# Kernel tuning notes

Measured on AMD Instinct MI355X. Metric: run time of the kernel, lower is better.

The kernel has to match this reference:

```python
import jax, jax.numpy as jnp
import numpy as np

B, T, A, C = 8, 512, 512, 8
D, NHEAD, FF, L = 256, 8, 1024, 3
DEC_FF = 512
V = 32          # categorical cardinality per feature (tables have 1+V rows, row 0 = padding)
NEG = -1e9      # finite stand-in for -inf: exp underflows to 0 exactly, masked rows are zeroed anyway


def layer_norm(x, g, b, eps=1e-5):
    m = jnp.mean(x, axis=-1, keepdims=True)
    v = jnp.mean(jnp.square(x - m), axis=-1, keepdims=True)
    return (x - m) * jax.lax.rsqrt(v + eps) * g + b


def mha(q_in, k_in, v_in, wq, wk, wv, wo, nhead, mask=None):
    b, _, dm = q_in.shape
    dh = dm // nhead
    # faithful to the original torch code: .view(B, nhead, -1, d_head) with NO transpose
    q = (q_in @ wq).reshape(b, nhead, -1, dh)
    k = (k_in @ wk).reshape(b, nhead, -1, dh)
    v = (v_in @ wv).reshape(b, nhead, -1, dh)
    u = jnp.einsum('bhqd,bhkd->bhqk', q, k) / float(np.sqrt(dh))
    if mask is not None:
        m = mask[:, None]  # [B,1,q,k] (broadcast)
        attn = jax.nn.softmax(jnp.where(m, NEG, u), axis=-1)
        attn = jnp.where(m, 0.0, attn)
    else:
        attn = jax.nn.softmax(u, axis=-1)
    return jnp.einsum('bhqk,bhkd->bhqd', attn, v).reshape(b, -1, dm) @ wo


def embed(x, tables, wo, bo):
    # all features categorical: Embedder sums per-feature embeddings of (1 + x), then a Linear
    nf = x.shape[-1]
    e = tables[jnp.arange(nf), 1 + x]  # [B,N,nf,D]
    return jnp.sum(e, axis=2) @ wo + bo


def encoder(x, mask, wq, wk, wv, wo, w1, b1, w2, b2, g1, be1, g2, be2):
    for i in range(wq.shape[0]):
        x = layer_norm(x + mha(x, x, x, wq[i], wk[i], wv[i], wo[i], NHEAD, mask), g1[i], be1[i])
        x = layer_norm(x + jax.nn.relu(x @ w1[i] + b1[i]) @ w2[i] + b2[i], g2[i], be2[i])
    return x


def forward(tasks, agents, indices, P):
    (emb_t, emb_t_wo, emb_t_bo, emb_a, emb_a_wo, emb_a_bo,
     et_wq, et_wk, et_wv, et_wo, et_w1, et_b1, et_w2, et_b2, et_g1, et_be1, et_g2, et_be2,
     ea_wq, ea_wk, ea_wv, ea_wo, ea_w1, ea_b1, ea_w2, ea_b2, ea_g1, ea_be1, ea_g2, ea_be2,
     de_wq, de_wk, de_wv, de_wo, de_w1, de_b1, de_w2, de_b2, de_g1, de_be1, de_g2, de_be2,
     do_wq, do_wk) = P
    padding_mask = jnp.all(tasks == -1, axis=-1)[:, None, :]  # [B,1,T]
    # _get_mask: scatter assigned task indices (slot 0 absorbs the -1 padding)
    b_idx = jnp.arange(B)[:, None, None]
    a_idx = jnp.arange(A)[None, :, None]
    am = jnp.zeros((B, A, 1 + T), jnp.bool_).at[b_idx, a_idx, 1 + indices].set(True)
    assignment_mask = jnp.any(am[..., 1:], axis=1, keepdims=True)      # [B,1,T]
    full_mask = jnp.all(indices != -1, axis=-1, keepdims=True)         # [B,A,1]
    mask = jnp.swapaxes(assignment_mask | padding_mask | full_mask, -1, -2)  # [B,T,A]
    ht = encoder(embed(tasks, emb_t, emb_t_wo, emb_t_bo), padding_mask,
                 et_wq, et_wk, et_wv, et_wo, et_w1, et_b1, et_w2, et_b2, et_g1, et_be1, et_g2, et_be2)
    ha = encoder(embed(agents, emb_a, emb_a_wo, emb_a_bo), padding_mask,
                 ea_wq, ea_wk, ea_wv, ea_wo, ea_w1, ea_b1, ea_w2, ea_b2, ea_g1, ea_be1, ea_g2, ea_be2)
    # decoder (x=ha, h=ht): queries are the task stream, keys/values the agent stream
    h = layer_norm(ht + mha(ht, ha, ha, de_wq, de_wk, de_wv, de_wo, NHEAD, mask), de_g1, de_be1)
    h = layer_norm(h + jax.nn.relu(h @ de_w1 + de_b1) @ de_w2 + de_b2, de_g2, de_be2)
    # output attention (nhead=1, d_head=D); mean over the singleton head dim is identity
    scores = jnp.einsum('btd,bad->bta', h @ do_wq, ha @ do_wk) / float(np.sqrt(D))
    probs = 8.0 * jnp.tanh(scores)                                     # [B,T,A]
    p = jax.nn.softmax(jnp.where(mask, NEG, probs), axis=-1)
    p = jnp.where(mask, 0.0, p)
    return jnp.swapaxes(p, -1, -2)                                     # [B,A,T]


def setup_inputs():
    key = jax.random.key(0)
    kc = iter(jax.random.split(key, 64))
    def w(*shape):
        return jax.random.normal(next(kc), shape, jnp.float32) * 0.05
    def table(nf):
        t = jax.random.normal(next(kc), (nf, 1 + V, D), jnp.float32) * 0.05
        return t.at[:, 0].set(0.0)  # padding_idx=0
    inp = {
        'tasks': jax.random.randint(next(kc), (B, T, 4), 0, V, jnp.int32),
        'agents': jax.random.randint(next(kc), (B, A, 2), 0, V, jnp.int32),
        'indices': jax.random.randint(next(kc), (B, A, C), 0, T + 1, jnp.int32) - 1,  # in [-1, T-1]
        'emb_t': table(4), 'emb_t_wo': w(D, D), 'emb_t_bo': jnp.zeros((D,), jnp.float32),
        'emb_a': table(2), 'emb_a_wo': w(D, D), 'emb_a_bo': jnp.zeros((D,), jnp.float32),
    }
    for pre in ('et', 'ea'):
        inp[pre + '_wq'] = w(L, D, D); inp[pre + '_wk'] = w(L, D, D)
        inp[pre + '_wv'] = w(L, D, D); inp[pre + '_wo'] = w(L, D, D)
        inp[pre + '_w1'] = w(L, D, FF); inp[pre + '_b1'] = jnp.zeros((L, FF), jnp.float32)
        inp[pre + '_w2'] = w(L, FF, D); inp[pre + '_b2'] = jnp.zeros((L, D), jnp.float32)
        inp[pre + '_g1'] = jnp.ones((L, D), jnp.float32); inp[pre + '_be1'] = jnp.zeros((L, D), jnp.float32)
        inp[pre + '_g2'] = jnp.ones((L, D), jnp.float32); inp[pre + '_be2'] = jnp.zeros((L, D), jnp.float32)
    inp['de_wq'] = w(D, D); inp['de_wk'] = w(D, D); inp['de_wv'] = w(D, D); inp['de_wo'] = w(D, D)
    inp['de_w1'] = w(D, DEC_FF); inp['de_b1'] = jnp.zeros((DEC_FF,), jnp.float32)
    inp['de_w2'] = w(DEC_FF, D); inp['de_b2'] = jnp.zeros((D,), jnp.float32)
    inp['de_g1'] = jnp.ones((D,), jnp.float32); inp['de_be1'] = jnp.zeros((D,), jnp.float32)
    inp['de_g2'] = jnp.ones((D,), jnp.float32); inp['de_be2'] = jnp.zeros((D,), jnp.float32)
    inp['do_wq'] = w(D, D); inp['do_wk'] = w(D, D)
    return inp


def reference(tasks, agents, indices, emb_t, emb_t_wo, emb_t_bo, emb_a, emb_a_wo, emb_a_bo,
              et_wq, et_wk, et_wv, et_wo, et_w1, et_b1, et_w2, et_b2, et_g1, et_be1, et_g2, et_be2,
              ea_wq, ea_wk, ea_wv, ea_wo, ea_w1, ea_b1, ea_w2, ea_b2, ea_g1, ea_be1, ea_g2, ea_be2,
              de_wq, de_wk, de_wv, de_wo, de_w1, de_b1, de_w2, de_b2, de_g1, de_be1, de_g2, de_be2,
              do_wq, do_wk):
    P = (emb_t, emb_t_wo, emb_t_bo, emb_a, emb_a_wo, emb_a_bo,
         et_wq, et_wk, et_wv, et_wo, et_w1, et_b1, et_w2, et_b2, et_g1, et_be1, et_g2, et_be2,
         ea_wq, ea_wk, ea_wv, ea_wo, ea_w1, ea_b1, ea_w2, ea_b2, ea_g1, ea_be1, ea_g2, ea_be2,
         de_wq, de_wk, de_wv, de_wo, de_w1, de_b1, de_w2, de_b2, de_g1, de_be1, de_g2, de_be2,
         do_wq, do_wk)
    return forward(tasks, agents, indices, P)
```

## Files before the change

kernel.cpp:

```cpp
#include <hip/hip_runtime.h>
#include <hip/hip_bf16.h>

constexpr int CB = 8;
constexpr int CT = 512;
constexpr int CA = 512;
constexpr int CC = 8;
constexpr int CD = 256;
constexpr float NEGV = -1.0e9f;

typedef __attribute__((ext_vector_type(8))) short bf16x8;
typedef __attribute__((ext_vector_type(4))) float f32x4;

__device__ inline short f2bf(float f) {
  uint32_t u = __float_as_uint(f);
  uint32_t r = (u + 0x7FFFu + ((u >> 16) & 1u)) >> 16;
  return (short)r;
}

__global__ void mask_prep_kernel(const int* __restrict__ tasks,
                                 const int* __restrict__ indices,
                                 int* __restrict__ asgn, int* __restrict__ fullm,
                                 int* __restrict__ padm) {
  int i = blockIdx.x * blockDim.x + threadIdx.x;
  if (i >= CB * CT) return;
  asgn[i] = 0;
  const int* tp = tasks + i * 4;
  padm[i] = (tp[0] == -1) && (tp[1] == -1) && (tp[2] == -1) && (tp[3] == -1);
  const int* ip = indices + i * CC;
  int full = 1;
#pragma unroll
  for (int c = 0; c < CC; ++c) full &= (ip[c] != -1);
  fullm[i] = full;
}

__global__ void mask_assign_kernel(const int* __restrict__ indices, int* __restrict__ asgn) {
  int i = blockIdx.x * blockDim.x + threadIdx.x;
  if (i >= CB * CA * CC) return;
  int b = i / (CA * CC);
  int idx = indices[i];
  if (idx >= 0) asgn[b * CT + idx] = 1;
}

struct TDesc { const float* src; short* dst; int K; int N; int tbase; };
struct TArgs { TDesc d[46]; int nd; };

__global__ __launch_bounds__(256) void trans_kernel(TArgs a) {
  __shared__ short Ts[64][72];
  const int bid = blockIdx.x;
  int w = 0;
#pragma unroll 1
  for (int i = 1; i < a.nd; ++i)
    if (a.d[i].tbase <= bid) w = i;
  const TDesc de = a.d[w];
  const int ti = bid - de.tbase;
  const int ntn = de.N >> 6;
  const int n0 = (ti % ntn) * 64, k0 = (ti / ntn) * 64;
  const int t = threadIdx.x;
  const int kk = t >> 4, c4 = (t & 15) * 4;
#pragma unroll
  for (int r = 0; r < 4; ++r) {
    float4 v = *(const float4*)(de.src + (size_t)(k0 + kk + r * 16) * de.N + n0 + c4);
    Ts[c4 + 0][kk + r * 16] = f2bf(v.x);
    Ts[c4 + 1][kk + r * 16] = f2bf(v.y);
    Ts[c4 + 2][kk + r * 16] = f2bf(v.z);
    Ts[c4 + 3][kk + r * 16] = f2bf(v.w);
  }
  __syncthreads();
  const int n = t >> 3, k8 = (t & 7) * 8;
#pragma unroll
  for (int r = 0; r < 2; ++r)
    *(bf16x8*)(de.dst + (size_t)(n0 + n + r * 32) * de.K + k0 + k8) =
        *(bf16x8*)&Ts[n + r * 32][k8];
}

__global__ void embed2_kernel(const int* __restrict__ tasks, const int* __restrict__ agents,
                              const float* __restrict__ tab_t, const float* __restrict__ tab_a,
                              short* __restrict__ out) {
  int row = blockIdx.x;
  int lane = threadIdx.x;
  const int* tp;
  const float* table;
  int nf;
  short* dst;
  if (row < 4096) {
    tp = tasks + row * 4; table = tab_t; nf = 4; dst = out + (size_t)row * CD;
  } else {
    int r = row - 4096;
    tp = agents + r * 2; table = tab_a; nf = 2; dst = out + 1048576 + (size_t)r * CD;
  }
  float4 acc = make_float4(0.f, 0.f, 0.f, 0.f);
  for (int f = 0; f < nf; ++f) {
    int t = 1 + tp[f];
    float4 v = *(const float4*)(table + ((size_t)f * 33 + t) * CD + lane * 4);
    acc.x += v.x; acc.y += v.y; acc.z += v.z; acc.w += v.w;
  }
  short4 o;
  o.x = f2bf(acc.x); o.y = f2bf(acc.y); o.z = f2bf(acc.z); o.w = f2bf(acc.w);
  *(short4*)(dst + lane * 4) = o;
}

__device__ __forceinline__ void ln_row(float* x, const float* res, const float* g,
                                       const float* b, short* xb, int row, int lane) {
  float4 xv = *(const float4*)(x + (size_t)row * CD + lane * 4);
  float4 rv = *(const float4*)(res + (size_t)row * CD + lane * 4);
  float v0 = xv.x + rv.x, v1 = xv.y + rv.y, v2 = xv.z + rv.z, v3 = xv.w + rv.w;
  float s = v0 + v1 + v2 + v3;
  float s2 = v0 * v0 + v1 * v1 + v2 * v2 + v3 * v3;
#pragma unroll
  for (int off = 32; off >= 1; off >>= 1) {
    s += __shfl_xor(s, off);
    s2 += __shfl_xor(s2, off);
  }
  float mean = s * (1.0f / CD);
  float var = s2 * (1.0f / CD) - mean * mean;
  float rstd = rsqrtf(var + 1e-5f);
  float4 gv = *(const float4*)(g + lane * 4);
  float4 bv = *(const float4*)(b + lane * 4);
  float4 o;
  o.x = (v0 - mean) * rstd * gv.x + bv.x;
  o.y = (v1 - mean) * rstd * gv.y + bv.y;
  o.z = (v2 - mean) * rstd * gv.z + bv.z;
  o.w = (v3 - mean) * rstd * gv.w + bv.w;
  *(float4*)(x + (size_t)row * CD + lane * 4) = o;
  short4 ob;
  ob.x = f2bf(o.x); ob.y = f2bf(o.y); ob.z = f2bf(o.z); ob.w = f2bf(o.w);
  *(short4*)(xb + (size_t)row * CD + lane * 4) = ob;
}

__global__ __launch_bounds__(256) void ln_add1_kernel(
    float* __restrict__ x, const float* __restrict__ res,
    const float* __restrict__ g, const float* __restrict__ b, short* __restrict__ xb) {
  int row = blockIdx.x * 4 + (threadIdx.x >> 6);
  ln_row(x, res, g, b, xb, row, threadIdx.x & 63);
}

__global__ __launch_bounds__(256) void ln_add2_kernel(
    float* __restrict__ x0, const float* __restrict__ r0, const float* __restrict__ g0,
    const float* __restrict__ b0, short* __restrict__ s0,
    float* __restrict__ x1, const float* __restrict__ r1, const float* __restrict__ g1,
    const float* __restrict__ b1, short* __restrict__ s1) {
  int row = blockIdx.x * 4 + (threadIdx.x >> 6);
  int lane = threadIdx.x & 63;
  if (row < 4096) ln_row(x0, r0, g0, b0, s0, row, lane);
  else ln_row(x1, r1, g1, b1, s1, row - 4096, lane);
}

template <int CMODE, bool BIAS, bool RELU>
__device__ __forceinline__ void gemm_body(
    const short* __restrict__ Ab, const short* __restrict__ Bb,
    const float* __restrict__ bias, float* __restrict__ Cf, short* __restrict__ Cbf,
    int Ndim, int Kdim, int bm, int bn) {
  __shared__ __align__(16) short As[2][128 * 64];
  __shared__ __align__(16) short Bs[2][64 * 64];
  const int t = threadIdx.x;
  const int lane = t & 63, wave = t >> 6;
  const int wm = wave * 32;
  const int fr = lane & 15, fs = lane >> 4;
  const int fr7 = fr & 7;

  const int srow = t >> 3;
  const int lc = (t & 7) ^ (srow & 7);
  const short* Asrc = Ab + (size_t)(bm + srow) * Kdim + lc * 8;
  const short* Bsrc = Bb + (size_t)(bn + srow) * Kdim + lc * 8;

  f32x4 acc[2][4] = {};

  auto stage = [&](int buf, int k0) {
#pragma unroll
    for (int r = 0; r < 4; ++r)
      __builtin_amdgcn_global_load_lds(
          (const __attribute__((address_space(1))) void*)(Asrc + (size_t)(r * 32) * Kdim + k0),
          (__attribute__((address_space(3))) void*)(&As[buf][r * 2048 + wave * 512]),
          16, 0, 0);
#pragma unroll
    for (int r = 0; r < 2; ++r)
      __builtin_amdgcn_global_load_lds(
          (const __attribute__((address_space(1))) void*)(Bsrc + (size_t)(r * 32) * Kdim + k0),
          (__attribute__((address_space(3))) void*)(&Bs[buf][r * 2048 + wave * 512]),
          16, 0, 0);
  };

  stage(0, 0);
  __syncthreads();
  int buf = 0;
#pragma unroll 1
  for (int k0 = 0; k0 < Kdim; k0 += 64) {
    if (k0 + 64 < Kdim) stage(buf ^ 1, k0 + 64);
    const short* A0 = &As[buf][(wm + fr) * 64];
    const short* A1 = &As[buf][(wm + 16 + fr) * 64];
    const short* B0 = &Bs[buf][fr * 64];
    const short* B1 = &Bs[buf][(16 + fr) * 64];
    const short* B2 = &Bs[buf][(32 + fr) * 64];
    const short* B3 = &Bs[buf][(48 + fr) * 64];
#pragma unroll
    for (int kk = 0; kk < 2; ++kk) {
      const int co = (((kk * 4) + fs) ^ fr7) * 8;
      bf16x8 a0 = *(bf16x8*)(A0 + co);
      bf16x8 a1 = *(bf16x8*)(A1 + co);
      bf16x8 bf0 = *(bf16x8*)(B0 + co);
      bf16x8 bf1 = *(bf16x8*)(B1 + co);
      bf16x8 bf2 = *(bf16x8*)(B2 + co);
      bf16x8 bf3 = *(bf16x8*)(B3 + co);
      acc[0][0] = __builtin_amdgcn_mfma_f32_16x16x32_bf16(a0, bf0, acc[0][0], 0, 0, 0);
      acc[0][1] = __builtin_amdgcn_mfma_f32_16x16x32_bf16(a0, bf1, acc[0][1], 0, 0, 0);
      acc[0][2] = __builtin_amdgcn_mfma_f32_16x16x32_bf16(a0, bf2, acc[0][2], 0, 0, 0);
      acc[0][3] = __builtin_amdgcn_mfma_f32_16x16x32_bf16(a0, bf3, acc[0][3], 0, 0, 0);
      acc[1][0] = __builtin_amdgcn_mfma_f32_16x16x32_bf16(a1, bf0, acc[1][0], 0, 0, 0);
      acc[1][1] = __builtin_amdgcn_mfma_f32_16x16x32_bf16(a1, bf1, acc[1][1], 0, 0, 0);
      acc[1][2] = __builtin_amdgcn_mfma_f32_16x16x32_bf16(a1, bf2, acc[1][2], 0, 0, 0);
      acc[1][3] = __builtin_amdgcn_mfma_f32_16x16x32_bf16(a1, bf3, acc[1][3], 0, 0, 0);
    }
    __syncthreads();
    buf ^= 1;
  }

#pragma unroll
  for (int fi = 0; fi < 2; ++fi)
#pragma unroll
    for (int fj = 0; fj < 4; ++fj) {
      int row0 = bm + wm + fi * 16 + fs * 4;
      int col = bn + fj * 16 + fr;
      float bv = BIAS ? bias[col] : 0.0f;
#pragma unroll
      for (int r = 0; r < 4; ++r) {
        float v = acc[fi][fj][r] + bv;
        if (RELU) v = fmaxf(v, 0.0f);
        if (CMODE == 0 || CMODE == 2) Cf[(size_t)(row0 + r) * Ndim + col] = v;
        if (CMODE == 1 || CMODE == 2) Cbf[(size_t)(row0 + r) * Ndim + col] = f2bf(v);
      }
    }
}

struct GArgs {
  const short* A[8];
  const short* Bm[8];
  const float* bias[8];
  float* Cf[8];
  short* Cb[8];
  int Ndim, Kdim;
};

template <int CMODE, bool BIAS, bool RELU>
__global__ __launch_bounds__(256) void mgemm_kernel(GArgs ga) {
  int z = blockIdx.z;
  gemm_body<CMODE, BIAS, RELU>(ga.A[z], ga.Bm[z], ga.bias[z], ga.Cf[z], ga.Cb[z],
                               ga.Ndim, ga.Kdim, blockIdx.x * 128, blockIdx.y * 64);
}

template <int MODE>
__global__ __launch_bounds__(512) void mattn_kernel(
    const short* __restrict__ qb, const short* __restrict__ kb, const short* __restrict__ vb,
    short* __restrict__ ob,
    const int* __restrict__ asgn, const int* __restrict__ fullm, const int* __restrict__ padm) {
  __shared__ short Ks[512][40];
  __shared__ short Vt[32][520];
  __shared__ short Pb[8][16][40];
  __shared__ unsigned int mwords[16];
  const int bh = blockIdx.x;
  const int b = (bh >> 3) & 7;
  const size_t base = (size_t)bh * (512 * 32);
  const int tid = threadIdx.x;

#pragma unroll
  for (int r = 0; r < 4; ++r) {
    int i = r * 512 + tid;
    int row = i >> 2, seg = (i & 3) * 8;
    *(bf16x8*)&Ks[row][seg] = *(const bf16x8*)(kb + base + row * 32 + seg);
  }
  {
    int d = tid & 31, g = tid >> 5;
#pragma unroll
    for (int r = 0; r < 8; ++r) {
      int key0 = (r * 16 + g) * 4;
      const short* vp = vb + base + (size_t)key0 * 32 + d;
      unsigned short p0 = (unsigned short)vp[0];
      unsigned short p1 = (unsigned short)vp[32];
      unsigned short p2 = (unsigned short)vp[64];
      unsigned short p3 = (unsigned short)vp[96];
      int lo = ((int)p0) | (((int)p1) << 16);
      int hi = ((int)p2) | (((int)p3) << 16);
      *(int2*)&Vt[d][key0] = make_int2(lo, hi);
    }
  }
  if (tid < 16) {
    unsigned w = 0;
    for (int tl = 0; tl < 32; ++tl) {
      int key = tl * 16 + tid;
      int m = (MODE == 0) ? padm[b * CT + key] : fullm[b * CA + key];
      w |= ((unsigned)(m != 0)) << tl;
    }
    mwords[tid] = w;
  }
  __syncthreads();

  const int wave = tid >> 6, lane = tid & 63;
  const int fr = lane & 15, fs = lane >> 4;
  const int q0 = blockIdx.y * 128 + wave * 16;
  const int q = q0 + fr;

  bf16x8 qf = *(const bf16x8*)(qb + base + (size_t)q * 32 + fs * 8);

  unsigned qmbits = 0;
  if (MODE == 1) {
    int qm = asgn[b * CT + q] | padm[b * CT + q];
    qmbits = qm ? 0xFFFFFFFFu : 0u;
  }
  unsigned mw[4];
#pragma unroll
  for (int g = 0; g < 4; ++g) mw[g] = mwords[4 * fs + g] | qmbits;

  f32x4 s[32];
#pragma unroll
  for (int tl = 0; tl < 32; ++tl) {
    bf16x8 kf = *(bf16x8*)&Ks[tl * 16 + fr][fs * 8];
    f32x4 z = {0.f, 0.f, 0.f, 0.f};
    s[tl] = __builtin_amdgcn_mfma_f32_16x16x32_bf16(kf, qf, z, 0, 0, 0);
  }
  const float sc = 0.17677669529663687f;
  float mx = -3.0e38f;
#pragma unroll
  for (int tl = 0; tl < 32; ++tl)
#pragma unroll
    for (int g = 0; g < 4; ++g) mx = fmaxf(mx, s[tl][g]);
  mx = fmaxf(mx, __shfl_xor(mx, 16));
  mx = fmaxf(mx, __shfl_xor(mx, 32));
  float sum = 0.f;
#pragma unroll
  for (int tl = 0; tl < 32; ++tl)
#pragma unroll
    for (int g = 0; g < 4; ++g) {
      float e = __expf((s[tl][g] - mx) * sc);
      e = ((mw[g] >> tl) & 1u) ? 0.0f : e;
      s[tl][g] = e;
      sum += e;
    }
  sum += __shfl_xor(sum, 16);
  sum += __shfl_xor(sum, 32);
  float inv = (sum > 0.f) ? (1.0f / sum) : 0.0f;

  f32x4 o0 = {0.f, 0.f, 0.f, 0.f}, o1 = {0.f, 0.f, 0.f, 0.f};
#pragma unroll
  for (int c = 0; c < 16; ++c) {
    int w0, w1, w2, w3;
    asm("v_cvt_pk_bf16_f32 %0, %1, %2" : "=v"(w0) : "v"(s[2 * c][0]), "v"(s[2 * c][1]));
    asm("v_cvt_pk_bf16_f32 %0, %1, %2" : "=v"(w1) : "v"(s[2 * c][2]), "v"(s[2 * c][3]));
    asm("v_cvt_pk_bf16_f32 %0, %1, %2" : "=v"(w2) : "v"(s[2 * c + 1][0]), "v"(s[2 * c + 1][1]));
    asm("v_cvt_pk_bf16_f32 %0, %1, %2" : "=v"(w3) : "v"(s[2 * c + 1][2]), "v"(s[2 * c + 1][3]));
    *(int2*)&Pb[wave][fr][4 * fs] = make_int2(w0, w1);
    *(int2*)&Pb[wave][fr][16 + 4 * fs] = make_int2(w2, w3);
    asm volatile("s_waitcnt lgkmcnt(0)" ::: "memory");
    __builtin_amdgcn_sched_barrier(0);
    bf16x8 af = *(bf16x8*)&Pb[wave][fr][8 * fs];
    bf16x8 v0 = *(bf16x8*)&Vt[fr][32 * c + 8 * fs];
    bf16x8 v1 = *(bf16x8*)&Vt[16 + fr][32 * c + 8 * fs];
    o0 = __builtin_amdgcn_mfma_f32_16x16x32_bf16(af, v0, o0, 0, 0, 0);
    o1 = __builtin_amdgcn_mfma_f32_16x16x32_bf16(af, v1, o1, 0, 0, 0);
  }
#pragma unroll
  for (int g = 0; g < 4; ++g) {
    float iv = __shfl(inv, fs * 4 + g);
    int qq = q0 + fs * 4 + g;
    ob[base + (size_t)qq * 32 + fr] = f2bf(o0[g] * iv);
    ob[base + (size_t)qq * 32 + 16 + fr] = f2bf(o1[g] * iv);
  }
}

__global__ void final_kernel(const float* __restrict__ scores,
                             const int* __restrict__ asgn, const int* __restrict__ fullm,
                             const int* __restrict__ padm, float* __restrict__ out) {
  int row = blockIdx.x;
  int b = row >> 9, t = row & 511;
  int lane = threadIdx.x;
  int qm = asgn[row] | padm[row];
  const float* sp = scores + (size_t)row * 512;
  float v[8];
  int mk[8];
#pragma unroll
  for (int m = 0; m < 8; ++m) {
    int a = lane + (m << 6);
    float val = 8.0f * tanhf(sp[a] * (1.0f / 16.0f));
    int masked = qm | fullm[b * CA + a];
    mk[m] = masked;
    v[m] = masked ? NEGV : val;
  }
  float mx = v[0];
#pragma unroll
  for (int m = 1; m < 8; ++m) mx = fmaxf(mx, v[m]);
#pragma unroll
  for (int off = 32; off >= 1; off >>= 1) mx = fmaxf(mx, __shfl_xor(mx, off));
  float sum = 0.f, e[8];
#pragma unroll
  for (int m = 0; m < 8; ++m) { e[m] = __expf(v[m] - mx); sum += e[m]; }
#pragma unroll
  for (int off = 32; off >= 1; off >>= 1) sum += __shfl_xor(sum, off);
  float inv = 1.0f / sum;
#pragma unroll
  for (int m = 0; m < 8; ++m) {
    int a = lane + (m << 6);
    float p = mk[m] ? 0.0f : e[m] * inv;
    out[(size_t)b * (CA * CT) + (size_t)a * CT + t] = p;
  }
}

extern "C" void kernel_launch(void* const* d_in, const int* in_sizes, int n_in,
                              void* d_out, int out_size, void* d_ws, size_t ws_size,
                              hipStream_t stream) {
  const int* tasks = (const int*)d_in[0];
  const int* agents = (const int*)d_in[1];
  const int* indices = (const int*)d_in[2];
  const float* emb_t = (const float*)d_in[3];
  const float* emb_t_wo = (const float*)d_in[4];
  const float* emb_t_bo = (const float*)d_in[5];
  const float* emb_a = (const float*)d_in[6];
  const float* emb_a_wo = (const float*)d_in[7];
  const float* emb_a_bo = (const float*)d_in[8];
  const float* de_wq = (const float*)d_in[33];
  const float* de_wk = (const float*)d_in[34];
  const float* de_wv = (const float*)d_in[35];
  const float* de_wo = (const float*)d_in[36];
  const float* de_w1 = (const float*)d_in[37];
  const float* de_b1 = (const float*)d_in[38];
  const float* de_w2 = (const float*)d_in[39];
  const float* de_b2 = (const float*)d_in[40];
  const float* de_g1 = (const float*)d_in[41];
  const float* de_be1 = (const float*)d_in[42];
  const float* de_g2 = (const float*)d_in[43];
  const float* de_be2 = (const float*)d_in[44];
  const float* do_wq = (const float*)d_in[45];
  const float* do_wk = (const float*)d_in[46];

  float* ws = (float*)d_ws;
  float* ht = ws + 0;
  float* ha = ws + 1048576;
  short* htb = (short*)(ws + 2097152);
  short* hab = (short*)(ws + 2621440);
  short* qall = (short*)(ws + 3145728);
  short* kall = (short*)(ws + 4194304);
  short* vall = (short*)(ws + 5242880);
  short* t1b = (short*)(ws + 6291456);
  float* scores = ws + 6291456;
  float* t2 = ws + 10485760;
  short* wT = (short*)(ws + 12582912);
  int* asgn = (int*)(ws + 15400000);
  int* fullm = asgn + 4096;
  int* padm = asgn + 8192;

  TArgs ta;
  int idx = 0, tb = 0;
  size_t doff = 0;
  short* Wp[46];
  auto addw = [&](const float* s, int K, int N) {
    Wp[idx] = wT + doff;
    ta.d[idx] = {s, wT + doff, K, N, tb};
    tb += (K >> 6) * (N >> 6);
    doff += (size_t)K * N;
    ++idx;
  };
  addw(emb_t_wo, 256, 256);
  addw(emb_a_wo, 256, 256);
  for (int enc = 0; enc < 2; ++enc) {
    int pb = enc ? 21 : 9;
    const float* wq = (const float*)d_in[pb + 0];
    const float* wk = (const float*)d_in[pb + 1];
    const float* wv = (const float*)d_in[pb + 2];
    const float* wo = (const float*)d_in[pb + 3];
    const float* w1 = (const float*)d_in[pb + 4];
    const float* w2 = (const float*)d_in[pb + 6];
    for (int l = 0; l < 3; ++l) {
      addw(wq + l * 65536, 256, 256);
      addw(wk + l * 65536, 256, 256);
      addw(wv + l * 65536, 256, 256);
      addw(wo + l * 65536, 256, 256);
    }
    for (int l = 0; l < 3; ++l) addw(w1 + l * 262144, 256, 1024);
    for (int l = 0; l < 3; ++l) addw(w2 + l * 262144, 1024, 256);
  }
  addw(de_wq, 256, 256);
  addw(de_wk, 256, 256);
  addw(de_wv, 256, 256);
  addw(de_wo, 256, 256);
  addw(de_w1, 256, 512);
  addw(de_w2, 512, 256);
  addw(do_wq, 256, 256);
  addw(do_wk, 256, 256);
  ta.nd = idx;

  mask_prep_kernel<<<16, 256, 0, stream>>>(tasks, indices, asgn, fullm, padm);
  mask_assign_kernel<<<128, 256, 0, stream>>>(indices, asgn);
  trans_kernel<<<tb, 256, 0, stream>>>(ta);

  GArgs ga{};

  embed2_kernel<<<8192, 64, 0, stream>>>(tasks, agents, emb_t, emb_a, t1b);
  ga.A[0] = t1b;            ga.Bm[0] = Wp[0]; ga.bias[0] = emb_t_bo; ga.Cf[0] = ht; ga.Cb[0] = htb;
  ga.A[1] = t1b + 1048576;  ga.Bm[1] = Wp[1]; ga.bias[1] = emb_a_bo; ga.Cf[1] = ha; ga.Cb[1] = hab;
  ga.Ndim = 256; ga.Kdim = 256;
  mgemm_kernel<2, true, false><<<dim3(32, 4, 2), 256, 0, stream>>>(ga);

  const float* b1t = (const float*)d_in[14];
  const float* b2t = (const float*)d_in[16];
  const float* g1t = (const float*)d_in[17];
  const float* be1t = (const float*)d_in[18];
  const float* g2t = (const float*)d_in[19];
  const float* be2t = (const float*)d_in[20];
  const float* b1a = (const float*)d_in[26];
  const float* b2a = (const float*)d_in[28];
  const float* g1a = (const float*)d_in[29];
  const float* be1a = (const float*)d_in[30];
  const float* g2a = (const float*)d_in[31];
  const float* be2a = (const float*)d_in[32];

  for (int l = 0; l < 3; ++l) {
    for (int j = 0; j < 3; ++j) {
      ga.A[j] = htb;     ga.Bm[j] = Wp[2 + l * 4 + j];
      ga.A[3 + j] = hab; ga.Bm[3 + j] = Wp[20 + l * 4 + j];
    }
    short* outs[6] = {qall, kall, vall, qall + 1048576, kall + 1048576, vall + 1048576};
    for (int j = 0; j < 6; ++j) ga.Cb[j] = outs[j];
    ga.Ndim = 256; ga.Kdim = 256;
    mgemm_kernel<1, false, false><<<dim3(32, 4, 6), 256, 0, stream>>>(ga);
    mattn_kernel<0><<<dim3(128, 4, 1), 512, 0, stream>>>(qall, kall, vall, t1b,
                                                         asgn, fullm, padm);
    ga.A[0] = t1b;           ga.Bm[0] = Wp[2 + l * 4 + 3];  ga.Cf[0] = t2;
    ga.A[1] = t1b + 1048576; ga.Bm[1] = Wp[20 + l * 4 + 3]; ga.Cf[1] = t2 + 1048576;
    ga.Ndim = 256; ga.Kdim = 256;
    mgemm_kernel<0, false, false><<<dim3(32, 4, 2), 256, 0, stream>>>(ga);
    ln_add2_kernel<<<2048, 256, 0, stream>>>(ht, t2, g1t + l * 256, be1t + l * 256, htb,
                                             ha, t2 + 1048576, g1a + l * 256, be1a + l * 256, hab);
    ga.A[0] = htb; ga.Bm[0] = Wp[14 + l]; ga.bias[0] = b1t + l * 1024; ga.Cb[0] = t1b;
    ga.A[1] = hab; ga.Bm[1] = Wp[32 + l]; ga.bias[1] = b1a + l * 1024; ga.Cb[1] = t1b + 4194304;
    ga.Ndim = 1024; ga.Kdim = 256;
    mgemm_kernel<1, true, true><<<dim3(32, 16, 2), 256, 0, stream>>>(ga);
    ga.A[0] = t1b;           ga.Bm[0] = Wp[17 + l]; ga.bias[0] = b2t + l * 256; ga.Cf[0] = t2;
    ga.A[1] = t1b + 4194304; ga.Bm[1] = Wp[35 + l]; ga.bias[1] = b2a + l * 256; ga.Cf[1] = t2 + 1048576;
    ga.Ndim = 256; ga.Kdim = 1024;
    mgemm_kernel<0, true, false><<<dim3(32, 4, 2), 256, 0, stream>>>(ga);
    ln_add2_kernel<<<2048, 256, 0, stream>>>(ht, t2, g2t + l * 256, be2t + l * 256, htb,
                                             ha, t2 + 1048576, g2a + l * 256, be2a + l * 256, hab);
  }

  ga.A[0] = htb; ga.Bm[0] = Wp[38]; ga.Cb[0] = qall;
  ga.A[1] = hab; ga.Bm[1] = Wp[39]; ga.Cb[1] = kall;
  ga.A[2] = hab; ga.Bm[2] = Wp[40]; ga.Cb[2] = vall;
  ga.Ndim = 256; ga.Kdim = 256;
  mgemm_kernel<1, false, false><<<dim3(32, 4, 3), 256, 0, stream>>>(ga);
  mattn_kernel<1><<<dim3(64, 4, 1), 512, 0, stream>>>(qall, kall, vall, t1b,
                                                      asgn, fullm, padm);
  ga.A[0] = t1b; ga.Bm[0] = Wp[41]; ga.Cf[0] = t2;
  ga.Ndim = 256; ga.Kdim = 256;
  mgemm_kernel<0, false, false><<<dim3(32, 4, 1), 256, 0, stream>>>(ga);
  ln_add1_kernel<<<1024, 256, 0, stream>>>(ht, t2, de_g1, de_be1, htb);
  ga.A[0] = htb; ga.Bm[0] = Wp[42]; ga.bias[0] = de_b1; ga.Cb[0] = t1b;
  ga.Ndim = 512; ga.Kdim = 256;
  mgemm_kernel<1, true, true><<<dim3(32, 8, 1), 256, 0, stream>>>(ga);
  ga.A[0] = t1b; ga.Bm[0] = Wp[43]; ga.bias[0] = de_b2; ga.Cf[0] = t2;
  ga.Ndim = 256; ga.Kdim = 512;
  mgemm_kernel<0, true, false><<<dim3(32, 4, 1), 256, 0, stream>>>(ga);
  ln_add1_kernel<<<1024, 256, 0, stream>>>(ht, t2, de_g2, de_be2, htb);

  ga.A[0] = htb; ga.Bm[0] = Wp[44]; ga.Cb[0] = qall;
  ga.A[1] = hab; ga.Bm[1] = Wp[45]; ga.Cb[1] = kall;
  ga.Ndim = 256; ga.Kdim = 256;
  mgemm_kernel<1, false, false><<<dim3(32, 4, 2), 256, 0, stream>>>(ga);
  for (int b = 0; b < 8; ++b) {
    ga.A[b] = qall + (size_t)b * 131072;
    ga.Bm[b] = kall + (size_t)b * 131072;
    ga.Cf[b] = scores + (size_t)b * 262144;
  }
  ga.Ndim = 512; ga.Kdim = 256;
  mgemm_kernel<0, false, false><<<dim3(4, 8, 8), 256, 0, stream>>>(ga);
  final_kernel<<<4096, 64, 0, stream>>>(scores, asgn, fullm, padm, (float*)d_out);
}
```

Baseline: 483.2 us.

## Fuse residual add and LayerNorm into output-projection and FFN2 GEMM epilogues

Adds a GEMM kernel whose blocks each cover 64 full rows of the 256-wide output. Its epilogue adds bias and the residual, computes the row LayerNorm with shuffles, and writes both the fp32 and bf16 activations. This replaces the separate GEMM-to-t2 and ln_add launches, removing the t2 round trip and several launches per layer. The trade-off is fewer blocks per launch (64 per problem instead of 128), a large LDS footprint for B tiles that may limit occupancy, and scalar, less coalesced epilogue stores.

```diff
diff --git a/kernel.cpp b/kernel.cpp
--- a/kernel.cpp
+++ b/kernel.cpp
@@ -97,52 +97,6 @@
   short4 o;
   o.x = f2bf(acc.x); o.y = f2bf(acc.y); o.z = f2bf(acc.z); o.w = f2bf(acc.w);
   *(short4*)(dst + lane * 4) = o;
-}
-
-__device__ __forceinline__ void ln_row(float* x, const float* res, const float* g,
-                                       const float* b, short* xb, int row, int lane) {
-  float4 xv = *(const float4*)(x + (size_t)row * CD + lane * 4);
-  float4 rv = *(const float4*)(res + (size_t)row * CD + lane * 4);
-  float v0 = xv.x + rv.x, v1 = xv.y + rv.y, v2 = xv.z + rv.z, v3 = xv.w + rv.w;
-  float s = v0 + v1 + v2 + v3;
-  float s2 = v0 * v0 + v1 * v1 + v2 * v2 + v3 * v3;
-#pragma unroll
-  for (int off = 32; off >= 1; off >>= 1) {
-    s += __shfl_xor(s, off);
-    s2 += __shfl_xor(s2, off);
-  }
-  float mean = s * (1.0f / CD);
-  float var = s2 * (1.0f / CD) - mean * mean;
-  float rstd = rsqrtf(var + 1e-5f);
-  float4 gv = *(const float4*)(g + lane * 4);
-  float4 bv = *(const float4*)(b + lane * 4);
-  float4 o;
-  o.x = (v0 - mean) * rstd * gv.x + bv.x;
-  o.y = (v1 - mean) * rstd * gv.y + bv.y;
-  o.z = (v2 - mean) * rstd * gv.z + bv.z;
-  o.w = (v3 - mean) * rstd * gv.w + bv.w;
-  *(float4*)(x + (size_t)row * CD + lane * 4) = o;
-  short4 ob;
-  ob.x = f2bf(o.x); ob.y = f2bf(o.y); ob.z = f2bf(o.z); ob.w = f2bf(o.w);
-  *(short4*)(xb + (size_t)row * CD + lane * 4) = ob;
-}
-
-__global__ __launch_bounds__(256) void ln_add1_kernel(
-    float* __restrict__ x, const float* __restrict__ res,
-    const float* __restrict__ g, const float* __restrict__ b, short* __restrict__ xb) {
-  int row = blockIdx.x * 4 + (threadIdx.x >> 6);
-  ln_row(x, res, g, b, xb, row, threadIdx.x & 63);
-}
-
-__global__ __launch_bounds__(256) void ln_add2_kernel(
-    float* __restrict__ x0, const float* __restrict__ r0, const float* __restrict__ g0,
-    const float* __restrict__ b0, short* __restrict__ s0,
-    float* __restrict__ x1, const float* __restrict__ r1, const float* __restrict__ g1,
-    const float* __restrict__ b1, short* __restrict__ s1) {
-  int row = blockIdx.x * 4 + (threadIdx.x >> 6);
-  int lane = threadIdx.x & 63;
-  if (row < 4096) ln_row(x0, r0, g0, b0, s0, row, lane);
-  else ln_row(x1, r1, g1, b1, s1, row - 4096, lane);
 }
 
 template <int CMODE, bool BIAS, bool RELU>
@@ -245,6 +199,123 @@
   int z = blockIdx.z;
   gemm_body<CMODE, BIAS, RELU>(ga.A[z], ga.Bm[z], ga.bias[z], ga.Cf[z], ga.Cb[z],
                                ga.Ndim, ga.Kdim, blockIdx.x * 128, blockIdx.y * 64);
+}
+
+struct LArgs {
+  const short* A[4];
+  const short* Bm[4];
+  const float* bias[4];
+  float* x[4];
+  short* xb[4];
+  const float* g[4];
+  const float* be[4];
+  int Kdim;
+};
+
+template <bool BIAS>
+__global__ __launch_bounds__(256) void mgemmln_kernel(LArgs la) {
+  const int z = blockIdx.z;
+  const short* __restrict__ Ab = la.A[z];
+  const short* __restrict__ Bb = la.Bm[z];
+  const int Kdim = la.Kdim;
+  const int bm = blockIdx.x * 64;
+  __shared__ __align__(16) short As[2][64 * 64];
+  __shared__ __align__(16) short Bs[2][256 * 64];
+  const int t = threadIdx.x;
+  const int lane = t & 63, wave = t >> 6;
+  const int fr = lane & 15, fs = lane >> 4;
+  const int fr7 = fr & 7;
+
+  const int srow = t >> 3;
+  const int lc = (t & 7) ^ (srow & 7);
+  const short* Asrc = Ab + (size_t)(bm + srow) * Kdim + lc * 8;
+  const short* Bsrc = Bb + (size_t)srow * Kdim + lc * 8;
+
+  f32x4 acc[16] = {};
+
+  auto stage = [&](int buf, int k0) {
+#pragma unroll
+    for (int r = 0; r < 2; ++r)
+      __builtin_amdgcn_global_load_lds(
+          (const __attribute__((address_space(1))) void*)(Asrc + (size_t)(r * 32) * Kdim + k0),
+          (__attribute__((address_space(3))) void*)(&As[buf][r * 2048 + wave * 512]),
+          16, 0, 0);
+#pragma unroll
+    for (int r = 0; r < 8; ++r)
+      __builtin_amdgcn_global_load_lds(
+          (const __attribute__((address_space(1))) void*)(Bsrc + (size_t)(r * 32) * Kdim + k0),
+          (__attribute__((address_space(3))) void*)(&Bs[buf][r * 2048 + wave * 512]),
+          16, 0, 0);
+  };
+
+  stage(0, 0);
+  __syncthreads();
+  int buf = 0;
+#pragma unroll 1
+  for (int k0 = 0; k0 < Kdim; k0 += 64) {
+    if (k0 + 64 < Kdim) stage(buf ^ 1, k0 + 64);
+    const short* A0 = &As[buf][(wave * 16 + fr) * 64];
+#pragma unroll
+    for (int kk = 0; kk < 2; ++kk) {
+      const int co = (((kk * 4) + fs) ^ fr7) * 8;
+      bf16x8 a0 = *(bf16x8*)(A0 + co);
+#pragma unroll
+      for (int fj = 0; fj < 16; ++fj) {
+        bf16x8 bfj = *(bf16x8*)(&Bs[buf][(fj * 16 + fr) * 64] + co);
+        acc[fj] = __builtin_amdgcn_mfma_f32_16x16x32_bf16(a0, bfj, acc[fj], 0, 0, 0);
+      }
+    }
+    __syncthreads();
+    buf ^= 1;
+  }
+
+  float* __restrict__ xf = la.x[z];
+  short* __restrict__ xb = la.xb[z];
+  const float* __restrict__ gp = la.g[z];
+  const float* __restrict__ bep = la.be[z];
+  const int rbase = bm + wave * 16 + fs * 4;
+#pragma unroll
+  for (int fj = 0; fj < 16; ++fj) {
+    int col = fj * 16 + fr;
+    float bv = BIAS ? la.bias[z][col] : 0.0f;
+#pragma unroll
+    for (int r = 0; r < 4; ++r)
+      acc[fj][r] += bv + xf[(size_t)(rbase + r) * 256 + col];
+  }
+  float s[4] = {0.f, 0.f, 0.f, 0.f}, s2[4] = {0.f, 0.f, 0.f, 0.f};
+#pragma unroll
+  for (int fj = 0; fj < 16; ++fj)
+#pragma unroll
+    for (int r = 0; r < 4; ++r) {
+      float u = acc[fj][r];
+      s[r] += u;
+      s2[r] += u * u;
+    }
+#pragma unroll
+  for (int off = 8; off >= 1; off >>= 1)
+#pragma unroll
+    for (int r = 0; r < 4; ++r) {
+      s[r] += __shfl_xor(s[r], off);
+      s2[r] += __shfl_xor(s2[r], off);
+    }
+  float mean[4], rstd[4];
+#pragma unroll
+  for (int r = 0; r < 4; ++r) {
+    mean[r] = s[r] * (1.0f / 256.0f);
+    float var = s2[r] * (1.0f / 256.0f) - mean[r] * mean[r];
+    rstd[r] = rsqrtf(var + 1e-5f);
+  }
+#pragma unroll
+  for (int fj = 0; fj < 16; ++fj) {
+    int col = fj * 16 + fr;
+    float gv = gp[col], bev = bep[col];
+#pragma unroll
+    for (int r = 0; r < 4; ++r) {
+      float o = (acc[fj][r] - mean[r]) * rstd[r] * gv + bev;
+      xf[(size_t)(rbase + r) * 256 + col] = o;
+      xb[(size_t)(rbase + r) * 256 + col] = f2bf(o);
+    }
+  }
 }
 
 template <int MODE>
@@ -439,7 +510,6 @@
   short* vall = (short*)(ws + 5242880);
   short* t1b = (short*)(ws + 6291456);
   float* scores = ws + 6291456;
-  float* t2 = ws + 10485760;
   short* wT = (short*)(ws + 12582912);
   int* asgn = (int*)(ws + 15400000);
   int* fullm = asgn + 4096;
@@ -490,6 +560,7 @@
   trans_kernel<<<tb, 256, 0, stream>>>(ta);
 
   GArgs ga{};
+  LArgs la{};
 
   embed2_kernel<<<8192, 64, 0, stream>>>(tasks, agents, emb_t, emb_a, t1b);
   ga.A[0] = t1b;            ga.Bm[0] = Wp[0]; ga.bias[0] = emb_t_bo; ga.Cf[0] = ht; ga.Cb[0] = htb;
@@ -521,22 +592,22 @@
     mgemm_kernel<1, false, false><<<dim3(32, 4, 6), 256, 0, stream>>>(ga);
     mattn_kernel<0><<<dim3(128, 4, 1), 512, 0, stream>>>(qall, kall, vall, t1b,
                                                          asgn, fullm, padm);
-    ga.A[0] = t1b;           ga.Bm[0] = Wp[2 + l * 4 + 3];  ga.Cf[0] = t2;
-    ga.A[1] = t1b + 1048576; ga.Bm[1] = Wp[20 + l * 4 + 3]; ga.Cf[1] = t2 + 1048576;
-    ga.Ndim = 256; ga.Kdim = 256;
-    mgemm_kernel<0, false, false><<<dim3(32, 4, 2), 256, 0, stream>>>(ga);
-    ln_add2_kernel<<<2048, 256, 0, stream>>>(ht, t2, g1t + l * 256, be1t + l * 256, htb,
-                                             ha, t2 + 1048576, g1a + l * 256, be1a + l * 256, hab);
+    la.A[0] = t1b;           la.Bm[0] = Wp[2 + l * 4 + 3];
+    la.A[1] = t1b + 1048576; la.Bm[1] = Wp[20 + l * 4 + 3];
+    la.x[0] = ht; la.xb[0] = htb; la.g[0] = g1t + l * 256; la.be[0] = be1t + l * 256;
+    la.x[1] = ha; la.xb[1] = hab; la.g[1] = g1a + l * 256; la.be[1] = be1a + l * 256;
+    la.Kdim = 256;
+    mgemmln_kernel<false><<<dim3(64, 1, 2), 256, 0, stream>>>(la);
     ga.A[0] = htb; ga.Bm[0] = Wp[14 + l]; ga.bias[0] = b1t + l * 1024; ga.Cb[0] = t1b;
     ga.A[1] = hab; ga.Bm[1] = Wp[32 + l]; ga.bias[1] = b1a + l * 1024; ga.Cb[1] = t1b + 4194304;
     ga.Ndim = 1024; ga.Kdim = 256;
     mgemm_kernel<1, true, true><<<dim3(32, 16, 2), 256, 0, stream>>>(ga);
-    ga.A[0] = t1b;           ga.Bm[0] = Wp[17 + l]; ga.bias[0] = b2t + l * 256; ga.Cf[0] = t2;
-    ga.A[1] = t1b + 4194304; ga.Bm[1] = Wp[35 + l]; ga.bias[1] = b2a + l * 256; ga.Cf[1] = t2 + 1048576;
-    ga.Ndim = 256; ga.Kdim = 1024;
-    mgemm_kernel<0, true, false><<<dim3(32, 4, 2), 256, 0, stream>>>(ga);
-    ln_add2_kernel<<<2048, 256, 0, stream>>>(ht, t2, g2t + l * 256, be2t + l * 256, htb,
-                                             ha, t2 + 1048576, g2a + l * 256, be2a + l * 256, hab);
+    la.A[0] = t1b;           la.Bm[0] = Wp[17 + l]; la.bias[0] = b2t + l * 256;
+    la.A[1] = t1b + 4194304; la.Bm[1] = Wp[35 + l]; la.bias[1] = b2a + l * 256;
+    la.x[0] = ht; la.xb[0] = htb; la.g[0] = g2t + l * 256; la.be[0] = be2t + l * 256;
+    la.x[1] = ha; la.xb[1] = hab; la.g[1] = g2a + l * 256; la.be[1] = be2a + l * 256;
+    la.Kdim = 1024;
+    mgemmln_kernel<true><<<dim3(64, 1, 2), 256, 0, stream>>>(la);
   }
 
   ga.A[0] = htb; ga.Bm[0] = Wp[38]; ga.Cb[0] = qall;
@@ -546,17 +617,17 @@
   mgemm_kernel<1, false, false><<<dim3(32, 4, 3), 256, 0, stream>>>(ga);
   mattn_kernel<1><<<dim3(64, 4, 1), 512, 0, stream>>>(qall, kall, vall, t1b,
                                                       asgn, fullm, padm);
-  ga.A[0] = t1b; ga.Bm[0] = Wp[41]; ga.Cf[0] = t2;
-  ga.Ndim = 256; ga.Kdim = 256;
-  mgemm_kernel<0, false, false><<<dim3(32, 4, 1), 256, 0, stream>>>(ga);
-  ln_add1_kernel<<<1024, 256, 0, stream>>>(ht, t2, de_g1, de_be1, htb);
+  la.A[0] = t1b; la.Bm[0] = Wp[41];
+  la.x[0] = ht; la.xb[0] = htb; la.g[0] = de_g1; la.be[0] = de_be1;
+  la.Kdim = 256;
+  mgemmln_kernel<false><<<dim3(64, 1, 1), 256, 0, stream>>>(la);
   ga.A[0] = htb; ga.Bm[0] = Wp[42]; ga.bias[0] = de_b1; ga.Cb[0] = t1b;
   ga.Ndim = 512; ga.Kdim = 256;
   mgemm_kernel<1, true, true><<<dim3(32, 8, 1), 256, 0, stream>>>(ga);
-  ga.A[0] = t1b; ga.Bm[0] = Wp[43]; ga.bias[0] = de_b2; ga.Cf[0] = t2;
-  ga.Ndim = 256; ga.Kdim = 512;
-  mgemm_kernel<0, true, false><<<dim3(32, 4, 1), 256, 0, stream>>>(ga);
-  ln_add1_kernel<<<1024, 256, 0, stream>>>(ht, t2, de_g2, de_be2, htb);
+  la.A[0] = t1b; la.Bm[0] = Wp[43]; la.bias[0] = de_b2;
+  la.x[0] = ht; la.xb[0] = htb; la.g[0] = de_g2; la.be[0] = de_be2;
+  la.Kdim = 512;
+  mgemmln_kernel<true><<<dim3(64, 1, 1), 256, 0, stream>>>(la);
 
   ga.A[0] = htb; ga.Bm[0] = Wp[44]; ga.Cb[0] = qall;
   ga.A[1] = hab; ga.Bm[1] = Wp[45]; ga.Cb[1] = kall;
```

Result: slower. 512.7 us (+6.1%).
